# Optimization experiments

Measured on AMD Instinct MI355X. Metric: run time of the kernel, lower is better.

## Reference

```python
import jax, jax.numpy as jnp
import numpy as np

N = 8192
E = 262144
NFEAT, NHID, NCLASS = 128, 256, 16


def setup_inputs() -> dict:
    key = jax.random.key(0)
    k = jax.random.split(key, 6)
    x = jax.random.normal(k[0], (N, NFEAT), dtype=jnp.float32)
    edge_index = jax.random.randint(k[1], (2, E), 0, N, dtype=jnp.int64)
    edge_weight = jax.random.uniform(k[2], (E,), dtype=jnp.float32)
    W1 = jax.random.normal(k[3], (NFEAT, NHID), dtype=jnp.float32) * (1.0 / np.sqrt(NFEAT))
    b1 = jnp.zeros((NHID,), dtype=jnp.float32)
    W2 = jax.random.normal(k[4], (NHID, NCLASS), dtype=jnp.float32) * (1.0 / np.sqrt(NHID))
    b2 = jnp.zeros((NCLASS,), dtype=jnp.float32)
    return {"x": x, "edge_index": edge_index, "edge_weight": edge_weight,
            "W1": W1, "b1": b1, "W2": W2, "b2": b2}


def _norm_adj(edge_index, edge_weight, num_nodes, dtype):
    # dense scatter-add adjacency (adj[row, col] += w), matching the torch code
    adj = jnp.zeros((num_nodes, num_nodes), dtype=dtype)
    adj = adj.at[edge_index[0], edge_index[1]].add(edge_weight)
    adj = adj + jnp.eye(num_nodes, dtype=dtype)  # self loops
    # degree computed under no_grad in the original -> stop_gradient here
    deg = jax.lax.stop_gradient(jnp.sum(adj, axis=1))
    dinv = jnp.where(deg > 0, deg ** -0.5, jnp.zeros_like(deg))  # inf -> 0
    # D^{-1/2} A D^{-1/2} (diag matmuls expressed as broadcasts, same math)
    return dinv[:, None] * adj * dinv[None, :]


def reference(x, edge_index, edge_weight, W1, b1, W2, b2):
    norm_adj = _norm_adj(edge_index, edge_weight, x.shape[0], x.dtype)
    # submodel: 2-layer GCN, relu(A X W1) -> A H W2 -> log_softmax
    h = jax.nn.relu(norm_adj @ (x @ W1) + b1)
    out = norm_adj @ (h @ W2) + b2
    return jax.nn.log_softmax(out, axis=-1)
```

## Files before the change

kernel.cpp:

```cpp
#include <hip/hip_runtime.h>
#include <math.h>

#define N_NODES 8192
#define N_EDGES 262144
#define NFEAT 128
#define NHID 256
#define NCLASS 16
#define ELLS 96


__device__ inline unsigned int f2bf(float f) {
    unsigned int u = __float_as_uint(f);
    u += 0x7fffu + ((u >> 16) & 1u);
    return u >> 16;
}

#define CVT4(v, f) { \
    f[0] = __uint_as_float((v).x << 16); f[1] = __uint_as_float((v).x & 0xffff0000u); \
    f[2] = __uint_as_float((v).y << 16); f[3] = __uint_as_float((v).y & 0xffff0000u); }

__global__ void zero_kernel(int* __restrict__ p) {
    p[blockIdx.x * 256 + threadIdx.x] = 0;
}

__global__ __launch_bounds__(256) void histscatter_kernel(const int* __restrict__ ei,
                                                          const float* __restrict__ ew,
                                                          int* __restrict__ cnt,
                                                          int2* __restrict__ ell) {
    int e = blockIdx.x * 256 + threadIdx.x;
    int r = ei[e];
    int c = ei[N_EDGES + e];
    float w = ew[e];
    int slot = atomicAdd(&cnt[r], 1);
    ell[r * ELLS + slot] = make_int2(c, __float_as_int(w));
}

__global__ __launch_bounds__(256) void dinvcvt_kernel(const int* __restrict__ cnt,
                                                      const int2* __restrict__ ell,
                                                      const float* __restrict__ x,
                                                      float* __restrict__ dinv,
                                                      uint4* __restrict__ xs) {
    int t = threadIdx.x;
    int j = t & 15;
    int r = blockIdx.x * 16 + (t >> 4);
    int n = cnt[r];
    float sum = 0.0f;
    for (int base = 0; base < n; base += 16) {
        int idx = base + j;
        if (idx < n) sum += __int_as_float(ell[r * ELLS + idx].y);
    }
    #pragma unroll
    for (int off = 1; off < 16; off <<= 1) sum += __shfl_xor(sum, off, 16);
    float di = rsqrtf(sum + 1.0f);
    if (j == 0) dinv[r] = di;
    const float4* xp = (const float4*)(x + (size_t)r * NFEAT + j * 8);
    float4 a = xp[0], b = xp[1];
    uint4 o;
    o.x = f2bf(di * a.x) | (f2bf(di * a.y) << 16);
    o.y = f2bf(di * a.z) | (f2bf(di * a.w) << 16);
    o.z = f2bf(di * b.x) | (f2bf(di * b.y) << 16);
    o.w = f2bf(di * b.z) | (f2bf(di * b.w) << 16);
    xs[r * 16 + j] = o;
}

__global__ __launch_bounds__(256) void layer12_kernel(const int* __restrict__ cnt,
                                                      const int2* __restrict__ ell,
                                                      const uint2* __restrict__ xs2,
                                                      const float* __restrict__ dinv,
                                                      const float* __restrict__ W1,
                                                      const float* __restrict__ b1,
                                                      const float* __restrict__ W2,
                                                      float* __restrict__ V2s) {
    __shared__ float axs[8][NFEAT];
    __shared__ float hs[8][NHID + 4];
    __shared__ float part[256];
    int t = threadIdx.x;

    int lane = t & 31;
    int rloc = t >> 5;
    int r = blockIdx.x * 8 + rloc;
    int n = cnt[r];
    float di = dinv[r];
    uint2 xv = xs2[r * 32 + lane];
    float acc[4];
    CVT4(xv, acc);
    for (int base = 0; base < n; base += 16) {
        int idx = base + (lane & 15);
        int2 cw = ell[r * ELLS + idx];
        int cc = cw.x & (N_NODES - 1);
        float wl = __int_as_float(cw.y);
        wl = (idx < n) ? wl : 0.0f;
        #pragma unroll
        for (int u = 0; u < 16; ++u) {
            int c = __shfl(cc, u, 16);
            float w = __shfl(wl, u, 16);
            uint2 v = xs2[c * 32 + lane];
            float vf[4]; CVT4(v, vf);
            #pragma unroll
            for (int i = 0; i < 4; ++i) acc[i] += w * vf[i];
        }
    }
    #pragma unroll
    for (int i = 0; i < 4; ++i) acc[i] *= di;
    ((float4*)&axs[rloc][lane * 4])[0] = make_float4(acc[0], acc[1], acc[2], acc[3]);
    __syncthreads();

    float hacc[8];
    #pragma unroll
    for (int q = 0; q < 8; ++q) hacc[q] = 0.0f;
    #pragma unroll 4
    for (int k = 0; k < NFEAT; ++k) {
        float w = W1[k * NHID + t];
        #pragma unroll
        for (int q = 0; q < 8; ++q) hacc[q] += axs[q][k] * w;
    }
    float bb = b1[t];
    #pragma unroll
    for (int q = 0; q < 8; ++q) {
        float v = hacc[q] + bb;
        hs[q][t] = v > 0.0f ? v : 0.0f;
    }
    __syncthreads();

    int j = t & 15;
    int rq = (t >> 4) & 7;
    int kb = (t >> 7) * 128;
    float p = 0.0f;
    #pragma unroll 8
    for (int k = 0; k < 128; ++k) p += hs[rq][kb + k] * W2[(kb + k) * NCLASS + j];
    part[t] = p;
    __syncthreads();
    if (t < 128) {
        int rg = blockIdx.x * 8 + (t >> 4);
        V2s[rg * NCLASS + (t & 15)] = dinv[rg] * (part[t] + part[t + 128]);
    }
}

__global__ __launch_bounds__(256) void agg2_kernel(const int* __restrict__ cnt,
                                                   const int2* __restrict__ ell,
                                                   const float* __restrict__ V2s,
                                                   const float* __restrict__ dinv,
                                                   const float* __restrict__ b2,
                                                   float* __restrict__ out) {
    int t = threadIdx.x;
    int j = t & 15;
    int r = blockIdx.x * 16 + (t >> 4);
    int n = cnt[r];
    float di = dinv[r];
    float acc = V2s[r * NCLASS + j];
    for (int base = 0; base < n; base += 16) {
        int idx = base + j;
        int2 cw = ell[r * ELLS + idx];
        int cc = cw.x & (N_NODES - 1);
        float wl = __int_as_float(cw.y);
        wl = (idx < n) ? wl : 0.0f;
        #pragma unroll
        for (int u = 0; u < 16; ++u) {
            int c = __shfl(cc, u, 16);
            float w = __shfl(wl, u, 16);
            acc += w * V2s[c * NCLASS + j];
        }
    }
    float v = di * acc + b2[j];
    float mx = v;
    #pragma unroll
    for (int off = 1; off < 16; off <<= 1) mx = fmaxf(mx, __shfl_xor(mx, off));
    float ex = expf(v - mx);
    float ssum = ex;
    #pragma unroll
    for (int off = 1; off < 16; off <<= 1) ssum += __shfl_xor(ssum, off);
    out[r * NCLASS + j] = v - mx - logf(ssum);
}

extern "C" void kernel_launch(void* const* d_in, const int* in_sizes, int n_in,
                              void* d_out, int out_size, void* d_ws, size_t ws_size,
                              hipStream_t stream) {
    const float* x  = (const float*)d_in[0];
    const int*   ei = (const int*)d_in[1];
    const float* ew = (const float*)d_in[2];
    const float* W1 = (const float*)d_in[3];
    const float* b1 = (const float*)d_in[4];
    const float* W2 = (const float*)d_in[5];
    const float* b2 = (const float*)d_in[6];
    float* out = (float*)d_out;

    const int n = N_NODES;

    char* ws = (char*)d_ws;
    int*   cnt  = (int*)  (ws);
    float* dinv = (float*)(ws + 32768);
    int2*  ell  = (int2*) (ws + 65536);
    float* V2s  = (float*)(ws + 8388608);
    uint4* xs   = (uint4*)(ws + 16777216);

    zero_kernel<<<32, 256, 0, stream>>>(cnt);

    histscatter_kernel<<<N_EDGES / 256, 256, 0, stream>>>(ei, ew, cnt, ell);
    dinvcvt_kernel<<<n / 16, 256, 0, stream>>>(cnt, ell, x, dinv, xs);

    layer12_kernel<<<n / 8, 256, 0, stream>>>(cnt, ell, (const uint2*)xs,
                                              dinv, W1, b1, W2, V2s);
    agg2_kernel<<<n / 16, 256, 0, stream>>>(cnt, ell, V2s, dinv, b2, out);
}
```

Baseline: 59.65 us.

## Widen per-row thread groups across dinv, layer12 and agg2 kernels

Result: no change. 59.67 us (+0.0%).

```diff
diff --git a/kernel.cpp b/kernel.cpp
--- a/kernel.cpp
+++ b/kernel.cpp
@@ -14,10 +14,8 @@
     u += 0x7fffu + ((u >> 16) & 1u);
     return u >> 16;
 }
-
-#define CVT4(v, f) { \
-    f[0] = __uint_as_float((v).x << 16); f[1] = __uint_as_float((v).x & 0xffff0000u); \
-    f[2] = __uint_as_float((v).y << 16); f[3] = __uint_as_float((v).y & 0xffff0000u); }
+__device__ inline float bf_lo(unsigned int u) { return __uint_as_float(u << 16); }
+__device__ inline float bf_hi(unsigned int u) { return __uint_as_float(u & 0xffff0000u); }
 
 __global__ void zero_kernel(int* __restrict__ p) {
     p[blockIdx.x * 256 + threadIdx.x] = 0;
@@ -39,51 +37,48 @@
                                                       const int2* __restrict__ ell,
                                                       const float* __restrict__ x,
                                                       float* __restrict__ dinv,
-                                                      uint4* __restrict__ xs) {
+                                                      uint2* __restrict__ xs) {
     int t = threadIdx.x;
-    int j = t & 15;
-    int r = blockIdx.x * 16 + (t >> 4);
+    int lane = t & 31;
+    int r = blockIdx.x * 8 + (t >> 5);
     int n = cnt[r];
     float sum = 0.0f;
-    for (int base = 0; base < n; base += 16) {
-        int idx = base + j;
+    for (int base = 0; base < n; base += 32) {
+        int idx = base + lane;
         if (idx < n) sum += __int_as_float(ell[r * ELLS + idx].y);
     }
     #pragma unroll
-    for (int off = 1; off < 16; off <<= 1) sum += __shfl_xor(sum, off, 16);
+    for (int off = 1; off < 32; off <<= 1) sum += __shfl_xor(sum, off, 32);
     float di = rsqrtf(sum + 1.0f);
-    if (j == 0) dinv[r] = di;
-    const float4* xp = (const float4*)(x + (size_t)r * NFEAT + j * 8);
-    float4 a = xp[0], b = xp[1];
-    uint4 o;
+    if (lane == 0) dinv[r] = di;
+    float4 a = ((const float4*)(x + (size_t)r * NFEAT + lane * 4))[0];
+    uint2 o;
     o.x = f2bf(di * a.x) | (f2bf(di * a.y) << 16);
     o.y = f2bf(di * a.z) | (f2bf(di * a.w) << 16);
-    o.z = f2bf(di * b.x) | (f2bf(di * b.y) << 16);
-    o.w = f2bf(di * b.z) | (f2bf(di * b.w) << 16);
-    xs[r * 16 + j] = o;
-}
-
-__global__ __launch_bounds__(256) void layer12_kernel(const int* __restrict__ cnt,
+    xs[r * 32 + lane] = o;
+}
+
+__global__ __launch_bounds__(512) void layer12_kernel(const int* __restrict__ cnt,
                                                       const int2* __restrict__ ell,
-                                                      const uint2* __restrict__ xs2,
+                                                      const unsigned int* __restrict__ xs1,
                                                       const float* __restrict__ dinv,
                                                       const float* __restrict__ W1,
                                                       const float* __restrict__ b1,
                                                       const float* __restrict__ W2,
                                                       float* __restrict__ V2s) {
     __shared__ float axs[8][NFEAT];
+    __shared__ float psum[8][NHID];
     __shared__ float hs[8][NHID + 4];
-    __shared__ float part[256];
+    __shared__ float part[512];
     int t = threadIdx.x;
 
-    int lane = t & 31;
-    int rloc = t >> 5;
+    int lane = t & 63;
+    int rloc = t >> 6;
     int r = blockIdx.x * 8 + rloc;
     int n = cnt[r];
     float di = dinv[r];
-    uint2 xv = xs2[r * 32 + lane];
-    float acc[4];
-    CVT4(xv, acc);
+    unsigned int xv = xs1[r * 64 + lane];
+    float acc0 = bf_lo(xv), acc1 = bf_hi(xv);
     for (int base = 0; base < n; base += 16) {
         int idx = base + (lane & 15);
         int2 cw = ell[r * ELLS + idx];
@@ -94,45 +89,53 @@
         for (int u = 0; u < 16; ++u) {
             int c = __shfl(cc, u, 16);
             float w = __shfl(wl, u, 16);
-            uint2 v = xs2[c * 32 + lane];
-            float vf[4]; CVT4(v, vf);
-            #pragma unroll
-            for (int i = 0; i < 4; ++i) acc[i] += w * vf[i];
+            unsigned int v = xs1[c * 64 + lane];
+            acc0 += w * bf_lo(v);
+            acc1 += w * bf_hi(v);
         }
     }
-    #pragma unroll
-    for (int i = 0; i < 4; ++i) acc[i] *= di;
-    ((float4*)&axs[rloc][lane * 4])[0] = make_float4(acc[0], acc[1], acc[2], acc[3]);
-    __syncthreads();
-
+    ((float2*)&axs[rloc][lane * 2])[0] = make_float2(di * acc0, di * acc1);
+    __syncthreads();
+
+    int col = t & 255;
+    int kh = t >> 8;
     float hacc[8];
     #pragma unroll
     for (int q = 0; q < 8; ++q) hacc[q] = 0.0f;
+    int k0 = kh * 64;
     #pragma unroll 4
-    for (int k = 0; k < NFEAT; ++k) {
-        float w = W1[k * NHID + t];
+    for (int k = k0; k < k0 + 64; ++k) {
+        float w = W1[k * NHID + col];
         #pragma unroll
         for (int q = 0; q < 8; ++q) hacc[q] += axs[q][k] * w;
     }
-    float bb = b1[t];
-    #pragma unroll
-    for (int q = 0; q < 8; ++q) {
-        float v = hacc[q] + bb;
-        hs[q][t] = v > 0.0f ? v : 0.0f;
+    if (kh == 0) {
+        #pragma unroll
+        for (int q = 0; q < 8; ++q) psum[q][col] = hacc[q];
+    }
+    __syncthreads();
+    if (kh == 1) {
+        float bb = b1[col];
+        #pragma unroll
+        for (int q = 0; q < 8; ++q) {
+            float v = psum[q][col] + hacc[q] + bb;
+            hs[q][col] = v > 0.0f ? v : 0.0f;
+        }
     }
     __syncthreads();
 
     int j = t & 15;
     int rq = (t >> 4) & 7;
-    int kb = (t >> 7) * 128;
+    int kb = (t >> 7) * 64;
     float p = 0.0f;
     #pragma unroll 8
-    for (int k = 0; k < 128; ++k) p += hs[rq][kb + k] * W2[(kb + k) * NCLASS + j];
+    for (int k = 0; k < 64; ++k) p += hs[rq][kb + k] * W2[(kb + k) * NCLASS + j];
     part[t] = p;
     __syncthreads();
     if (t < 128) {
         int rg = blockIdx.x * 8 + (t >> 4);
-        V2s[rg * NCLASS + (t & 15)] = dinv[rg] * (part[t] + part[t + 128]);
+        V2s[rg * NCLASS + (t & 15)] =
+            dinv[rg] * (part[t] + part[t + 128] + part[t + 256] + part[t + 384]);
     }
 }
 
@@ -143,12 +146,14 @@
                                                    const float* __restrict__ b2,
                                                    float* __restrict__ out) {
     int t = threadIdx.x;
-    int j = t & 15;
-    int r = blockIdx.x * 16 + (t >> 4);
+    int lane = t & 31;
+    int g = lane >> 4;
+    int j = lane & 15;
+    int r = blockIdx.x * 8 + (t >> 5);
     int n = cnt[r];
     float di = dinv[r];
-    float acc = V2s[r * NCLASS + j];
-    for (int base = 0; base < n; base += 16) {
+    float acc = (g == 0) ? V2s[r * NCLASS + j] : 0.0f;
+    for (int base = g * 16; base < n; base += 32) {
         int idx = base + j;
         int2 cw = ell[r * ELLS + idx];
         int cc = cw.x & (N_NODES - 1);
@@ -161,6 +166,7 @@
             acc += w * V2s[c * NCLASS + j];
         }
     }
+    acc += __shfl_xor(acc, 16, 32);
     float v = di * acc + b2[j];
     float mx = v;
     #pragma unroll
@@ -169,7 +175,7 @@
     float ssum = ex;
     #pragma unroll
     for (int off = 1; off < 16; off <<= 1) ssum += __shfl_xor(ssum, off);
-    out[r * NCLASS + j] = v - mx - logf(ssum);
+    if (g == 0) out[r * NCLASS + j] = v - mx - logf(ssum);
 }
 
 extern "C" void kernel_launch(void* const* d_in, const int* in_sizes, int n_in,
@@ -191,14 +197,14 @@
     float* dinv = (float*)(ws + 32768);
     int2*  ell  = (int2*) (ws + 65536);
     float* V2s  = (float*)(ws + 8388608);
-    uint4* xs   = (uint4*)(ws + 16777216);
+    uint2* xs   = (uint2*)(ws + 16777216);
 
     zero_kernel<<<32, 256, 0, stream>>>(cnt);
 
     histscatter_kernel<<<N_EDGES / 256, 256, 0, stream>>>(ei, ew, cnt, ell);
-    dinvcvt_kernel<<<n / 16, 256, 0, stream>>>(cnt, ell, x, dinv, xs);
-
-    layer12_kernel<<<n / 8, 256, 0, stream>>>(cnt, ell, (const uint2*)xs,
+    dinvcvt_kernel<<<n / 8, 256, 0, stream>>>(cnt, ell, x, dinv, xs);
+
+    layer12_kernel<<<n / 8, 512, 0, stream>>>(cnt, ell, (const unsigned int*)xs,
                                               dinv, W1, b1, W2, V2s);
-    agg2_kernel<<<n / 16, 256, 0, stream>>>(cnt, ell, V2s, dinv, b2, out);
-}
+    agg2_kernel<<<n / 8, 256, 0, stream>>>(cnt, ell, V2s, dinv, b2, out);
+}
```
